# Kernel optimization log

Measured on AMD Instinct MI355X. Metric: run time of the kernel, lower is better.

## Reference

```python
import jax, jax.numpy as jnp
import numpy as np

NEG_SLOPE = 0.2
RECON_W = 0.1
BN_EPS = 1e-5


def gat_conv(x, edge_index, W, a_src, a_dst, b):
    """PyG-style GATConv (eval mode, add_self_loops=True, concat heads).
    x: [N, F_in], W: [F_in, H*C], a_src/a_dst: [H, C], b: [H*C]."""
    N = x.shape[0]
    H, C = a_src.shape
    h = (x @ W).reshape(N, H, C)                      # [N,H,C]
    loop = jnp.arange(N, dtype=edge_index.dtype)
    src = jnp.concatenate([edge_index[0], loop])
    dst = jnp.concatenate([edge_index[1], loop])
    alpha_src = jnp.sum(h * a_src, axis=-1)           # [N,H]
    alpha_dst = jnp.sum(h * a_dst, axis=-1)           # [N,H]
    e = jax.nn.leaky_relu(alpha_src[src] + alpha_dst[dst], NEG_SLOPE)  # [E,H]
    # segment softmax over incoming edges of each destination node
    m = jax.ops.segment_max(e, dst, num_segments=N)
    e = jnp.exp(e - m[dst])
    s = jax.ops.segment_sum(e, dst, num_segments=N)
    p = e / s[dst]                                    # [E,H]
    out = jax.ops.segment_sum(p[:, :, None] * h[src], dst, num_segments=N)  # [N,H,C]
    return out.reshape(N, H * C) + b


def setup_inputs() -> dict:
    key = jax.random.key(0)
    ks = jax.random.split(key, 24)
    N, E = 100000, 800000
    F_in, hid, heads, n_cls, ctx_d, expl_d = 128, 32, 4, 10, 6, 32
    HC = hid * heads  # 128
    g = lambda k, shp, sc=0.1: jax.random.normal(k, shp, dtype=jnp.float32) * sc
    return {
        "x": jax.random.normal(ks[0], (N, F_in), dtype=jnp.float32),
        "edge_index": jax.random.randint(ks[1], (2, E), 0, N, dtype=jnp.int32),
        "context": jax.random.normal(ks[2], (N, ctx_d), dtype=jnp.float32),
        # GATConv 1: F_in -> hid, heads
        "W1": g(ks[3], (F_in, HC)), "a_src1": g(ks[4], (heads, hid)),
        "a_dst1": g(ks[5], (heads, hid)), "b1": g(ks[6], (HC,)),
        # BatchNorm1d(HC), eval mode
        "bn_gamma": jnp.ones((HC,), jnp.float32), "bn_beta": g(ks[7], (HC,)),
        "bn_mean": g(ks[8], (HC,)), "bn_var": jax.random.uniform(ks[9], (HC,), jnp.float32, 0.5, 1.5),
        # GATConv 2: HC -> hid, 1 head
        "W2": g(ks[10], (HC, hid)), "a_src2": g(ks[11], (1, hid)),
        "a_dst2": g(ks[12], (1, hid)), "b2": g(ks[13], (hid,)),
        # Reasoner MLP: ctx_d -> hid -> expl_d
        "rw1": g(ks[14], (ctx_d, hid)), "rb1": g(ks[15], (hid,)),
        "rw2": g(ks[16], (hid, expl_d)), "rb2": g(ks[17], (expl_d,)),
        # Decoder: expl_d -> hid
        "dw": g(ks[18], (expl_d, hid)), "db": g(ks[19], (hid,)),
        # Classifier: hid -> n_cls
        "cw": g(ks[20], (hid, n_cls)), "cb": g(ks[21], (n_cls,)),
    }


def reference(x, edge_index, context, W1, a_src1, a_dst1, b1,
              bn_gamma, bn_beta, bn_mean, bn_var,
              W2, a_src2, a_dst2, b2, rw1, rb1, rw2, rb2, dw, db, cw, cb):
    # layer 1: GAT -> BN(eval) -> ELU (dropout inactive in eval)
    h = gat_conv(x, edge_index, W1, a_src1, a_dst1, b1)
    h = (h - bn_mean) * jax.lax.rsqrt(bn_var + BN_EPS) * bn_gamma + bn_beta
    h = jax.nn.elu(h)
    # layer 2: GAT (1 head)
    h = gat_conv(h, edge_index, W2, a_src2, a_dst2, b2)  # [N, hid]
    # reasoner + decoder
    expl = jnp.maximum(context @ rw1 + rb1, 0.0) @ rw2 + rb2   # [N, expl_d]
    recon = expl @ dw + db                                     # [N, hid]
    combined = h + RECON_W * recon
    logits = combined @ cw + cb
    return jax.nn.log_softmax(logits, axis=1), expl
```

## Files before the change

### kernel.cpp

```cpp
#include <hip/hip_runtime.h>
#include <hip/hip_bf16.h>
#include <math.h>

#define NEG_SLOPE 0.2f
#define RECON_W 0.1f
#define BN_EPS 1e-5f
#define CAP 64

typedef __attribute__((ext_vector_type(8))) short short8;
typedef __attribute__((ext_vector_type(4))) float f32x4;

__device__ __forceinline__ float lrelu(float v) {
    return (v >= 0.f) ? v : NEG_SLOPE * v;
}
__device__ __forceinline__ unsigned short f2bf(float f) {
    unsigned int u = __float_as_uint(f);
    u = (u + 0x7fffu + ((u >> 16) & 1u)) >> 16;
    return (unsigned short)u;
}
__device__ __forceinline__ float bf2f(unsigned short u) {
    return __uint_as_float(((unsigned int)u) << 16);
}
__device__ __forceinline__ unsigned int pack2bf(float a, float b) {
    return (unsigned int)f2bf(a) | ((unsigned int)f2bf(b) << 16);
}
__device__ __forceinline__ void unpack2(unsigned int u, float& a, float& b) {
    a = bf2f((unsigned short)u);
    b = bf2f((unsigned short)(u >> 16));
}

__global__ void bucket_kernel(const int* __restrict__ src, const int* __restrict__ dst, int E,
                              int* __restrict__ cnt, int* __restrict__ csrS) {
    int e = blockIdx.x * blockDim.x + threadIdx.x;
    if (e >= E) return;
    int s = src[e], d = dst[e];
    int pos = atomicAdd(&cnt[d], 1);
    if (pos < CAP) csrS[(size_t)d * CAP + pos] = s;
}

__global__ __launch_bounds__(256) void prep_kernel(
    const float* __restrict__ W1, const float* __restrict__ W2,
    const float* __restrict__ b1, const float* __restrict__ g,
    const float* __restrict__ be, const float* __restrict__ m, const float* __restrict__ v,
    unsigned short* __restrict__ w1t, unsigned short* __restrict__ w2t,
    float* __restrict__ bnsc, float* __restrict__ bnsh) {
    int b = blockIdx.x, tid = threadIdx.x;
    if (b < 64) {
        int e = b * 256 + tid;
        w1t[e] = f2bf(W1[(e & 127) * 128 + (e >> 7)]);
    } else {
        #pragma unroll
        for (int it = 0; it < 16; it++) {
            int e = it * 256 + tid;
            w2t[e] = f2bf(W2[(e & 127) * 32 + (e >> 7)]);
        }
        if (tid < 128) {
            float s = rsqrtf(v[tid] + BN_EPS) * g[tid];
            bnsc[tid] = s;
            bnsh[tid] = (b1[tid] - m[tid]) * s + be[tid];
        }
    }
}

__global__ __launch_bounds__(256) void gemm1_mfma_kernel(
    const float* __restrict__ x, const unsigned short* __restrict__ w1t,
    const float* __restrict__ a_src, const float* __restrict__ a_dst,
    unsigned short* __restrict__ h1g, float* __restrict__ as1, float* __restrict__ ad1, int N) {
    __shared__ unsigned short sA[64 * 128];
    __shared__ unsigned short sBt[128 * 128];
    __shared__ float s_as[128], s_ad[128];
    int tid = threadIdx.x;
    int rowBase = blockIdx.x * 64;

    if (tid < 128) { s_as[tid] = a_src[tid]; s_ad[tid] = a_dst[tid]; }
    #pragma unroll
    for (int u = 0; u < 8; u++) {
        int f = tid + u * 256;
        int r = f >> 5, cg = f & 31;
        int gr = rowBase + r;
        float4 vv = make_float4(0.f, 0.f, 0.f, 0.f);
        if (gr < N) vv = *(const float4*)(x + (size_t)gr * 128 + cg * 4);
        uint2 pk;
        pk.x = pack2bf(vv.x, vv.y);
        pk.y = pack2bf(vv.z, vv.w);
        ((uint2*)sA)[f] = pk;
    }
    #pragma unroll
    for (int u = 0; u < 8; u++) {
        int f = tid + u * 256;
        ((uint4*)sBt)[f] = ((const uint4*)w1t)[f];
    }
    __syncthreads();

    int lane = tid & 63;
    int w = tid >> 6;
    int quad = lane >> 4;
    int m16 = lane & 15;

    f32x4 acc[8];
    #pragma unroll
    for (int t = 0; t < 8; t++) acc[t] = (f32x4){0.f, 0.f, 0.f, 0.f};

    #pragma unroll
    for (int kc = 0; kc < 4; kc++) {
        int k0 = kc * 32 + quad * 8;
        short8 af = *(const short8*)(sA + ((w * 16 + m16) * 128 + k0));
        #pragma unroll
        for (int t = 0; t < 8; t++) {
            short8 bf = *(const short8*)(sBt + ((t * 16 + m16) * 128 + k0));
            acc[t] = __builtin_amdgcn_mfma_f32_16x16x32_bf16(af, bf, acc[t], 0, 0, 0);
        }
    }

    #pragma unroll
    for (int t = 0; t < 8; t++) {
        #pragma unroll
        for (int r = 0; r < 4; r++) {
            int row = w * 16 + quad * 4 + r;
            int col = t * 16 + m16;
            sA[row * 128 + col] = f2bf(acc[t][r]);
        }
    }
    __syncthreads();
    #pragma unroll
    for (int u = 0; u < 8; u++) {
        int f = tid + u * 256;
        int r = f >> 5, cg = f & 31;
        int gr = rowBase + r;
        if (gr < N) *(uint2*)(h1g + (size_t)gr * 128 + cg * 4) = ((const uint2*)sA)[f];
    }
    {
        int row = tid >> 2, head = tid & 3;
        int gr = rowBase + row;
        if (gr < N) {
            const unsigned int* rowp = (const unsigned int*)(sA + row * 128);
            float ps = 0.f, pd = 0.f;
            #pragma unroll
            for (int j = 0; j < 16; j++) {
                float f0, f1;
                unpack2(rowp[head * 16 + j], f0, f1);
                int c = head * 32 + j * 2;
                ps = fmaf(f0, s_as[c], fmaf(f1, s_as[c + 1], ps));
                pd = fmaf(f0, s_ad[c], fmaf(f1, s_ad[c + 1], pd));
            }
            as1[gr * 4 + head] = ps;
            ad1[gr * 4 + head] = pd;
        }
    }
}

__global__ __launch_bounds__(256) void agg1_kernel(
    const unsigned short* __restrict__ h1g,
    const float* __restrict__ as1, const float* __restrict__ ad1,
    const int* __restrict__ cnt, const int* __restrict__ csrS,
    const float* __restrict__ bnscale, const float* __restrict__ bnshift,
    unsigned short* __restrict__ h1p, int N) {
    __shared__ int   sSrc[4][CAP + 2];
    __shared__ float sW[4][CAP + 2][4];
    int tid = threadIdx.x;
    int wid = tid >> 6;
    int lane = tid & 63;
    int n = (int)(((unsigned)blockIdx.x * blockDim.x + tid) >> 6);
    bool alive = (n < N);
    int total = 1;

    if (alive) {
        int deg = min(cnt[n], CAP);
        total = deg + 1;
        float4 ad4 = *(const float4*)(ad1 + (size_t)n * 4);
        if (lane <= deg) {
            int s = (lane < deg) ? csrS[n * CAP + lane] : n;
            float4 a = *(const float4*)(as1 + (size_t)s * 4);
            sSrc[wid][lane] = s;
            float4 w4;
            w4.x = __expf(lrelu(a.x + ad4.x));
            w4.y = __expf(lrelu(a.y + ad4.y));
            w4.z = __expf(lrelu(a.z + ad4.z));
            w4.w = __expf(lrelu(a.w + ad4.w));
            *(float4*)(&sW[wid][lane][0]) = w4;
        }
        if (deg == CAP && lane == 63) {
            float4 a = *(const float4*)(as1 + (size_t)n * 4);
            sSrc[wid][CAP] = n;
            float4 w4;
            w4.x = __expf(lrelu(a.x + ad4.x));
            w4.y = __expf(lrelu(a.y + ad4.y));
            w4.z = __expf(lrelu(a.z + ad4.z));
            w4.w = __expf(lrelu(a.w + ad4.w));
            *(float4*)(&sW[wid][CAP][0]) = w4;
        }
    }
    __syncthreads();
    if (!alive) return;

    int half = lane >> 5;
    int l = lane & 31;
    int hl = l >> 3;
    unsigned choff = (unsigned)(l << 2);
    const int* sS = sSrc[wid];
    const float* sWp = &sW[wid][0][0];

    float p0a = 0.f, p1a = 0.f, p2a = 0.f, p3a = 0.f, sa = 0.f;
    float p0b = 0.f, p1b = 0.f, p2b = 0.f, p3b = 0.f, sb = 0.f;
    int j = half;
    for (; j + 2 < total; j += 4) {
        int s0 = sS[j];
        int s1 = sS[j + 2];
        float w0 = sWp[(j << 2) + hl];
        float w1 = sWp[((j + 2) << 2) + hl];
        uint2 u0 = *(const uint2*)(h1g + (((unsigned)s0 << 7) + choff));
        uint2 u1 = *(const uint2*)(h1g + (((unsigned)s1 << 7) + choff));
        float f0, f1, f2, f3;
        unpack2(u0.x, f0, f1); unpack2(u0.y, f2, f3);
        p0a = fmaf(w0, f0, p0a); p1a = fmaf(w0, f1, p1a);
        p2a = fmaf(w0, f2, p2a); p3a = fmaf(w0, f3, p3a);
        sa += w0;
        unpack2(u1.x, f0, f1); unpack2(u1.y, f2, f3);
        p0b = fmaf(w1, f0, p0b); p1b = fmaf(w1, f1, p1b);
        p2b = fmaf(w1, f2, p2b); p3b = fmaf(w1, f3, p3b);
        sb += w1;
    }
    if (j < total) {
        int s0 = sS[j];
        float w0 = sWp[(j << 2) + hl];
        uint2 u0 = *(const uint2*)(h1g + (((unsigned)s0 << 7) + choff));
        float f0, f1, f2, f3;
        unpack2(u0.x, f0, f1); unpack2(u0.y, f2, f3);
        p0a = fmaf(w0, f0, p0a); p1a = fmaf(w0, f1, p1a);
        p2a = fmaf(w0, f2, p2a); p3a = fmaf(w0, f3, p3a);
        sa += w0;
    }
    float acc0 = p0a + p0b, acc1 = p1a + p1b, acc2 = p2a + p2b, acc3 = p3a + p3b;
    float ss = sa + sb;
    acc0 += __shfl_xor(acc0, 32); acc1 += __shfl_xor(acc1, 32);
    acc2 += __shfl_xor(acc2, 32); acc3 += __shfl_xor(acc3, 32);
    ss += __shfl_xor(ss, 32);
    if (half == 0) {
        float inv = 1.f / ss;
        float4 sc = *(const float4*)(bnscale + l * 4);
        float4 sh = *(const float4*)(bnshift + l * 4);
        float o0 = fmaf(acc0 * inv, sc.x, sh.x);
        float o1 = fmaf(acc1 * inv, sc.y, sh.y);
        float o2 = fmaf(acc2 * inv, sc.z, sh.z);
        float o3 = fmaf(acc3 * inv, sc.w, sh.w);
        o0 = (o0 > 0.f) ? o0 : expm1f(o0);
        o1 = (o1 > 0.f) ? o1 : expm1f(o1);
        o2 = (o2 > 0.f) ? o2 : expm1f(o2);
        o3 = (o3 > 0.f) ? o3 : expm1f(o3);
        uint2 pk;
        pk.x = pack2bf(o0, o1);
        pk.y = pack2bf(o2, o3);
        *(uint2*)(h1p + (size_t)n * 128 + l * 4) = pk;
    }
}

__global__ __launch_bounds__(256) void gemm2_mfma_kernel(
    const unsigned short* __restrict__ A, const unsigned short* __restrict__ w2t,
    const float* __restrict__ a_src, const float* __restrict__ a_dst,
    unsigned short* __restrict__ h2g, float* __restrict__ as2, float* __restrict__ ad2, int N) {
    __shared__ unsigned short sA[64 * 128];
    __shared__ unsigned short sBt[32 * 128];
    __shared__ unsigned short sC[64 * 32];
    __shared__ float s_as[32], s_ad[32];
    int tid = threadIdx.x;
    int rowBase = blockIdx.x * 64;

    if (tid < 32) { s_as[tid] = a_src[tid]; s_ad[tid] = a_dst[tid]; }
    #pragma unroll
    for (int u = 0; u < 4; u++) {
        int f = tid + u * 256;
        int r = f >> 4, g = f & 15;
        int gr = rowBase + r;
        uint4 vv = make_uint4(0, 0, 0, 0);
        if (gr < N) vv = *(const uint4*)(A + (size_t)gr * 128 + g * 8);
        ((uint4*)sA)[f] = vv;
    }
    #pragma unroll
    for (int u = 0; u < 2; u++) {
        int f = tid + u * 256;
        ((uint4*)sBt)[f] = ((const uint4*)w2t)[f];
    }
    __syncthreads();

    int lane = tid & 63;
    int w = tid >> 6;
    int quad = lane >> 4;
    int m16 = lane & 15;

    f32x4 acc[2];
    acc[0] = (f32x4){0.f, 0.f, 0.f, 0.f};
    acc[1] = (f32x4){0.f, 0.f, 0.f, 0.f};
    #pragma unroll
    for (int kc = 0; kc < 4; kc++) {
        int k0 = kc * 32 + quad * 8;
        short8 af = *(const short8*)(sA + ((w * 16 + m16) * 128 + k0));
        #pragma unroll
        for (int t = 0; t < 2; t++) {
            short8 bf = *(const short8*)(sBt + ((t * 16 + m16) * 128 + k0));
            acc[t] = __builtin_amdgcn_mfma_f32_16x16x32_bf16(af, bf, acc[t], 0, 0, 0);
        }
    }
    #pragma unroll
    for (int t = 0; t < 2; t++) {
        #pragma unroll
        for (int r = 0; r < 4; r++) {
            int row = w * 16 + quad * 4 + r;
            sC[row * 32 + t * 16 + m16] = f2bf(acc[t][r]);
        }
    }
    __syncthreads();
    {
        int r = tid >> 2, g = tid & 3;
        int gr = rowBase + r;
        if (gr < N) *(uint4*)(h2g + (size_t)gr * 32 + g * 8) = ((const uint4*)sC)[tid];
    }
    if (tid < 64) {
        int gr = rowBase + tid;
        if (gr < N) {
            const unsigned int* rowp = (const unsigned int*)(sC + tid * 32);
            float ps = 0.f, pd = 0.f;
            #pragma unroll
            for (int j = 0; j < 16; j++) {
                float f0, f1;
                unpack2(rowp[j], f0, f1);
                ps = fmaf(f0, s_as[j * 2], fmaf(f1, s_as[j * 2 + 1], ps));
                pd = fmaf(f0, s_ad[j * 2], fmaf(f1, s_ad[j * 2 + 1], pd));
            }
            as2[gr] = ps;
            ad2[gr] = pd;
        }
    }
}

__global__ __launch_bounds__(256) void agg2_kernel(
    const unsigned short* __restrict__ h2g,
    const float* __restrict__ as2, const float* __restrict__ ad2,
    const int* __restrict__ cnt, const int* __restrict__ csrS,
    const float* __restrict__ b2, float* __restrict__ hl2, int N) {
    __shared__ int   sSrc[4][CAP + 2];
    __shared__ float sW[4][CAP + 2];
    int tid = threadIdx.x;
    int wid = tid >> 6;
    int lane = tid & 63;
    int n = (int)(((unsigned)blockIdx.x * blockDim.x + tid) >> 6);
    bool alive = (n < N);
    int total = 1;

    if (alive) {
        int deg = min(cnt[n], CAP);
        total = deg + 1;
        float ad = ad2[n];
        if (lane <= deg) {
            int s = (lane < deg) ? csrS[n * CAP + lane] : n;
            sSrc[wid][lane] = s;
            sW[wid][lane] = __expf(lrelu(as2[s] + ad));
        }
        if (deg == CAP && lane == 63) {
            sSrc[wid][CAP] = n;
            sW[wid][CAP] = __expf(lrelu(as2[n] + ad));
        }
    }
    __syncthreads();
    if (!alive) return;

    int q = lane >> 4;
    int l = lane & 15;
    unsigned choff = (unsigned)(l << 1);
    const int* sS = sSrc[wid];
    const float* sWp = sW[wid];

    float a0a = 0.f, a1a = 0.f, sa = 0.f;
    float a0b = 0.f, a1b = 0.f, sb = 0.f;
    int j = q;
    for (; j + 4 < total; j += 8) {
        int s0 = sS[j];
        int s1 = sS[j + 4];
        float w0 = sWp[j];
        float w1 = sWp[j + 4];
        unsigned int u0 = *(const unsigned int*)(h2g + (((unsigned)s0 << 5) + choff));
        unsigned int u1 = *(const unsigned int*)(h2g + (((unsigned)s1 << 5) + choff));
        float f0, f1;
        unpack2(u0, f0, f1);
        a0a = fmaf(w0, f0, a0a); a1a = fmaf(w0, f1, a1a); sa += w0;
        unpack2(u1, f0, f1);
        a0b = fmaf(w1, f0, a0b); a1b = fmaf(w1, f1, a1b); sb += w1;
    }
    if (j < total) {
        int s0 = sS[j];
        float w0 = sWp[j];
        unsigned int u0 = *(const unsigned int*)(h2g + (((unsigned)s0 << 5) + choff));
        float f0, f1;
        unpack2(u0, f0, f1);
        a0a = fmaf(w0, f0, a0a); a1a = fmaf(w0, f1, a1a); sa += w0;
    }
    float acc0 = a0a + a0b, acc1 = a1a + a1b, ss = sa + sb;
    acc0 += __shfl_xor(acc0, 16); acc1 += __shfl_xor(acc1, 16); ss += __shfl_xor(ss, 16);
    acc0 += __shfl_xor(acc0, 32); acc1 += __shfl_xor(acc1, 32); ss += __shfl_xor(ss, 32);
    if (lane < 16) {
        float inv = 1.f / ss;
        float2 o = make_float2(acc0 * inv + b2[l * 2], acc1 * inv + b2[l * 2 + 1]);
        *(float2*)(hl2 + (size_t)n * 32 + l * 2) = o;
    }
}

__global__ __launch_bounds__(256) void head_kernel(
    const float* __restrict__ context, const float* __restrict__ hl2,
    const float* __restrict__ rw1, const float* __restrict__ rb1,
    const float* __restrict__ rw2, const float* __restrict__ rb2,
    const float* __restrict__ dw, const float* __restrict__ db,
    const float* __restrict__ cw, const float* __restrict__ cb,
    float* __restrict__ out_lsm, float* __restrict__ out_expl, int N) {
    __shared__ float s_rw1[192], s_rw2[1024], s_dw[1024], s_cw[320];
    __shared__ float s_rb1[32], s_rb2[32], s_db[32], s_cb[10];
    int tid = threadIdx.x;
    for (int i = tid; i < 192; i += 256) s_rw1[i] = rw1[i];
    for (int i = tid; i < 1024; i += 256) { s_rw2[i] = rw2[i]; s_dw[i] = dw[i]; }
    for (int i = tid; i < 320; i += 256) s_cw[i] = cw[i];
    if (tid < 32) { s_rb1[tid] = rb1[tid]; s_rb2[tid] = rb2[tid]; s_db[tid] = db[tid]; }
    if (tid < 10) s_cb[tid] = cb[tid];
    __syncthreads();
    int n = blockIdx.x * 256 + tid;
    if (n >= N) return;

    float ctx[6];
    #pragma unroll
    for (int i = 0; i < 6; i++) ctx[i] = context[(size_t)n * 6 + i];

    float t1[32];
    #pragma unroll
    for (int c = 0; c < 32; c++) t1[c] = s_rb1[c];
    #pragma unroll
    for (int i = 0; i < 6; i++) {
        float s = ctx[i];
        #pragma unroll
        for (int c = 0; c < 32; c++) t1[c] = fmaf(s, s_rw1[i * 32 + c], t1[c]);
    }
    #pragma unroll
    for (int c = 0; c < 32; c++) t1[c] = fmaxf(t1[c], 0.f);

    float ex[32];
    #pragma unroll
    for (int c = 0; c < 32; c++) ex[c] = s_rb2[c];
    #pragma unroll
    for (int c = 0; c < 32; c++) {
        float s = t1[c];
        #pragma unroll
        for (int c2 = 0; c2 < 32; c2++) ex[c2] = fmaf(s, s_rw2[c * 32 + c2], ex[c2]);
    }
    #pragma unroll
    for (int c = 0; c < 32; c += 4)
        *(float4*)(out_expl + (size_t)n * 32 + c) = make_float4(ex[c], ex[c + 1], ex[c + 2], ex[c + 3]);

    float rec[32];
    #pragma unroll
    for (int k = 0; k < 32; k++) rec[k] = s_db[k];
    #pragma unroll
    for (int c = 0; c < 32; c++) {
        float s = ex[c];
        #pragma unroll
        for (int k = 0; k < 32; k++) rec[k] = fmaf(s, s_dw[c * 32 + k], rec[k]);
    }
    float comb[32];
    #pragma unroll
    for (int k = 0; k < 32; k += 4) {
        float4 h = *(const float4*)(hl2 + (size_t)n * 32 + k);
        comb[k] = h.x + RECON_W * rec[k];
        comb[k + 1] = h.y + RECON_W * rec[k + 1];
        comb[k + 2] = h.z + RECON_W * rec[k + 2];
        comb[k + 3] = h.w + RECON_W * rec[k + 3];
    }
    float lg[10];
    #pragma unroll
    for (int j = 0; j < 10; j++) lg[j] = s_cb[j];
    #pragma unroll
    for (int k = 0; k < 32; k++) {
        float s = comb[k];
        #pragma unroll
        for (int j = 0; j < 10; j++) lg[j] = fmaf(s, s_cw[k * 10 + j], lg[j]);
    }
    float mx = lg[0];
    #pragma unroll
    for (int j = 1; j < 10; j++) mx = fmaxf(mx, lg[j]);
    float se = 0.f;
    #pragma unroll
    for (int j = 0; j < 10; j++) se += expf(lg[j] - mx);
    float lse = mx + logf(se);
    #pragma unroll
    for (int j = 0; j < 10; j++) out_lsm[(size_t)n * 10 + j] = lg[j] - lse;
}

extern "C" void kernel_launch(void* const* d_in, const int* in_sizes, int n_in,
                              void* d_out, int out_size, void* d_ws, size_t ws_size,
                              hipStream_t stream) {
    const float* x    = (const float*)d_in[0];
    const int* ei     = (const int*)d_in[1];
    const float* ctx  = (const float*)d_in[2];
    const float* W1   = (const float*)d_in[3];
    const float* a_s1 = (const float*)d_in[4];
    const float* a_d1 = (const float*)d_in[5];
    const float* b1   = (const float*)d_in[6];
    const float* bn_g = (const float*)d_in[7];
    const float* bn_b = (const float*)d_in[8];
    const float* bn_m = (const float*)d_in[9];
    const float* bn_v = (const float*)d_in[10];
    const float* W2   = (const float*)d_in[11];
    const float* a_s2 = (const float*)d_in[12];
    const float* a_d2 = (const float*)d_in[13];
    const float* b2   = (const float*)d_in[14];
    const float* rw1  = (const float*)d_in[15];
    const float* rb1  = (const float*)d_in[16];
    const float* rw2  = (const float*)d_in[17];
    const float* rb2  = (const float*)d_in[18];
    const float* dw   = (const float*)d_in[19];
    const float* db   = (const float*)d_in[20];
    const float* cw   = (const float*)d_in[21];
    const float* cb   = (const float*)d_in[22];

    int N = in_sizes[0] / 128;
    int E = in_sizes[1] / 2;
    const int* esrc = ei;
    const int* edst = ei + E;

    char* w = (char*)d_ws;
    auto alloc = [&](size_t bytes) {
        void* p = (void*)w;
        w += (bytes + 255) & ~(size_t)255;
        return p;
    };
    unsigned short* h1g = (unsigned short*)alloc((size_t)N * 128 * 2);
    unsigned short* h1p = (unsigned short*)alloc((size_t)N * 128 * 2);
    float* as1  = (float*)alloc((size_t)N * 4 * 4);
    float* ad1  = (float*)alloc((size_t)N * 4 * 4);
    float* as2  = (float*)alloc((size_t)N * 4);
    float* ad2  = (float*)alloc((size_t)N * 4);
    int* cnt    = (int*)alloc((size_t)N * 4);
    int* csrS   = (int*)alloc((size_t)N * CAP * 4);
    float* bnsc = (float*)alloc(128 * 4);
    float* bnsh = (float*)alloc(128 * 4);
    unsigned short* w1t = (unsigned short*)alloc(128 * 128 * 2);
    unsigned short* w2t = (unsigned short*)alloc(32 * 128 * 2);
    unsigned short* h2g = h1g;
    float* hl2 = (float*)(h1g + (size_t)N * 32);

    float* out0 = (float*)d_out;
    float* out1 = out0 + (size_t)N * 10;

    hipMemsetAsync(cnt, 0, (size_t)N * 4, stream);

    bucket_kernel<<<(E + 255) / 256, 256, 0, stream>>>(esrc, edst, E, cnt, csrS);
    prep_kernel<<<65, 256, 0, stream>>>(W1, W2, b1, bn_g, bn_b, bn_m, bn_v,
                                        w1t, w2t, bnsc, bnsh);
    gemm1_mfma_kernel<<<(N + 63) / 64, 256, 0, stream>>>(x, w1t, a_s1, a_d1, h1g, as1, ad1, N);
    agg1_kernel<<<(N + 3) / 4, 256, 0, stream>>>(h1g, as1, ad1, cnt, csrS,
                                                 bnsc, bnsh, h1p, N);
    gemm2_mfma_kernel<<<(N + 63) / 64, 256, 0, stream>>>(h1p, w2t, a_s2, a_d2, h2g, as2, ad2, N);
    agg2_kernel<<<(N + 3) / 4, 256, 0, stream>>>(h2g, as2, ad2, cnt, csrS, b2, hl2, N);
    head_kernel<<<(N + 255) / 256, 256, 0, stream>>>(ctx, hl2, rw1, rb1, rw2, rb2,
                                                     dw, db, cw, cb, out0, out1, N);
}
```

Measured before the change: 338.6 us.

## Assign fewer lanes per node in GAT aggregation kernels with wider loads

Both aggregation kernels now map a small lane group to each destination node (16 lanes in layer one, 8 in layer two) rather than a full 64-lane wavefront. Each lane loads wider vectors (uint4 / uint2) and keeps more accumulators, which removes the cross-half shuffle reductions. Since the average degree is about 9, this is meant to cut idle lanes and per-node overhead. The cost is more registers per thread and a serial edge loop inside each group, which can diverge when degrees differ within a wavefront.

```diff
diff --git a/kernel.cpp b/kernel.cpp
--- a/kernel.cpp
+++ b/kernel.cpp
@@ -155,103 +155,102 @@
     const int* __restrict__ cnt, const int* __restrict__ csrS,
     const float* __restrict__ bnscale, const float* __restrict__ bnshift,
     unsigned short* __restrict__ h1p, int N) {
-    __shared__ int   sSrc[4][CAP + 2];
-    __shared__ float sW[4][CAP + 2][4];
+    __shared__ int   sSrc[16][CAP + 1];
+    __shared__ float sW[16][CAP + 1][4];
     int tid = threadIdx.x;
-    int wid = tid >> 6;
-    int lane = tid & 63;
-    int n = (int)(((unsigned)blockIdx.x * blockDim.x + tid) >> 6);
+    int nid = tid >> 4;
+    int l   = tid & 15;
+    int n = blockIdx.x * 16 + nid;
     bool alive = (n < N);
-    int total = 1;
+    int total = 0;
 
     if (alive) {
         int deg = min(cnt[n], CAP);
         total = deg + 1;
         float4 ad4 = *(const float4*)(ad1 + (size_t)n * 4);
-        if (lane <= deg) {
-            int s = (lane < deg) ? csrS[n * CAP + lane] : n;
+        for (int slot = l; slot < total; slot += 16) {
+            int s = (slot < deg) ? csrS[n * CAP + slot] : n;
+            sSrc[nid][slot] = s;
             float4 a = *(const float4*)(as1 + (size_t)s * 4);
-            sSrc[wid][lane] = s;
             float4 w4;
             w4.x = __expf(lrelu(a.x + ad4.x));
             w4.y = __expf(lrelu(a.y + ad4.y));
             w4.z = __expf(lrelu(a.z + ad4.z));
             w4.w = __expf(lrelu(a.w + ad4.w));
-            *(float4*)(&sW[wid][lane][0]) = w4;
-        }
-        if (deg == CAP && lane == 63) {
-            float4 a = *(const float4*)(as1 + (size_t)n * 4);
-            sSrc[wid][CAP] = n;
-            float4 w4;
-            w4.x = __expf(lrelu(a.x + ad4.x));
-            w4.y = __expf(lrelu(a.y + ad4.y));
-            w4.z = __expf(lrelu(a.z + ad4.z));
-            w4.w = __expf(lrelu(a.w + ad4.w));
-            *(float4*)(&sW[wid][CAP][0]) = w4;
+            *(float4*)(&sW[nid][slot][0]) = w4;
         }
     }
     __syncthreads();
     if (!alive) return;
 
-    int half = lane >> 5;
-    int l = lane & 31;
-    int hl = l >> 3;
-    unsigned choff = (unsigned)(l << 2);
-    const int* sS = sSrc[wid];
-    const float* sWp = &sW[wid][0][0];
-
-    float p0a = 0.f, p1a = 0.f, p2a = 0.f, p3a = 0.f, sa = 0.f;
-    float p0b = 0.f, p1b = 0.f, p2b = 0.f, p3b = 0.f, sb = 0.f;
-    int j = half;
-    for (; j + 2 < total; j += 4) {
+    int hl = l >> 2;
+    unsigned choff = (unsigned)(l << 3);
+    const int* sS = sSrc[nid];
+    const float* sWp = &sW[nid][0][0];
+
+    float pa0 = 0.f, pa1 = 0.f, pa2 = 0.f, pa3 = 0.f;
+    float pa4 = 0.f, pa5 = 0.f, pa6 = 0.f, pa7 = 0.f;
+    float pb0 = 0.f, pb1 = 0.f, pb2 = 0.f, pb3 = 0.f;
+    float pb4 = 0.f, pb5 = 0.f, pb6 = 0.f, pb7 = 0.f;
+    float sa = 0.f, sb = 0.f;
+    int j = 0;
+    for (; j + 1 < total; j += 2) {
         int s0 = sS[j];
-        int s1 = sS[j + 2];
+        int s1 = sS[j + 1];
         float w0 = sWp[(j << 2) + hl];
-        float w1 = sWp[((j + 2) << 2) + hl];
-        uint2 u0 = *(const uint2*)(h1g + (((unsigned)s0 << 7) + choff));
-        uint2 u1 = *(const uint2*)(h1g + (((unsigned)s1 << 7) + choff));
-        float f0, f1, f2, f3;
-        unpack2(u0.x, f0, f1); unpack2(u0.y, f2, f3);
-        p0a = fmaf(w0, f0, p0a); p1a = fmaf(w0, f1, p1a);
-        p2a = fmaf(w0, f2, p2a); p3a = fmaf(w0, f3, p3a);
+        float w1 = sWp[((j + 1) << 2) + hl];
+        uint4 u0 = *(const uint4*)(h1g + (((unsigned)s0 << 7) + choff));
+        uint4 u1 = *(const uint4*)(h1g + (((unsigned)s1 << 7) + choff));
+        float f0, f1;
+        unpack2(u0.x, f0, f1); pa0 = fmaf(w0, f0, pa0); pa1 = fmaf(w0, f1, pa1);
+        unpack2(u0.y, f0, f1); pa2 = fmaf(w0, f0, pa2); pa3 = fmaf(w0, f1, pa3);
+        unpack2(u0.z, f0, f1); pa4 = fmaf(w0, f0, pa4); pa5 = fmaf(w0, f1, pa5);
+        unpack2(u0.w, f0, f1); pa6 = fmaf(w0, f0, pa6); pa7 = fmaf(w0, f1, pa7);
         sa += w0;
-        unpack2(u1.x, f0, f1); unpack2(u1.y, f2, f3);
-        p0b = fmaf(w1, f0, p0b); p1b = fmaf(w1, f1, p1b);
-        p2b = fmaf(w1, f2, p2b); p3b = fmaf(w1, f3, p3b);
+        unpack2(u1.x, f0, f1); pb0 = fmaf(w1, f0, pb0); pb1 = fmaf(w1, f1, pb1);
+        unpack2(u1.y, f0, f1); pb2 = fmaf(w1, f0, pb2); pb3 = fmaf(w1, f1, pb3);
+        unpack2(u1.z, f0, f1); pb4 = fmaf(w1, f0, pb4); pb5 = fmaf(w1, f1, pb5);
+        unpack2(u1.w, f0, f1); pb6 = fmaf(w1, f0, pb6); pb7 = fmaf(w1, f1, pb7);
         sb += w1;
     }
     if (j < total) {
         int s0 = sS[j];
         float w0 = sWp[(j << 2) + hl];
-        uint2 u0 = *(const uint2*)(h1g + (((unsigned)s0 << 7) + choff));
-        float f0, f1, f2, f3;
-        unpack2(u0.x, f0, f1); unpack2(u0.y, f2, f3);
-        p0a = fmaf(w0, f0, p0a); p1a = fmaf(w0, f1, p1a);
-        p2a = fmaf(w0, f2, p2a); p3a = fmaf(w0, f3, p3a);
+        uint4 u0 = *(const uint4*)(h1g + (((unsigned)s0 << 7) + choff));
+        float f0, f1;
+        unpack2(u0.x, f0, f1); pa0 = fmaf(w0, f0, pa0); pa1 = fmaf(w0, f1, pa1);
+        unpack2(u0.y, f0, f1); pa2 = fmaf(w0, f0, pa2); pa3 = fmaf(w0, f1, pa3);
+        unpack2(u0.z, f0, f1); pa4 = fmaf(w0, f0, pa4); pa5 = fmaf(w0, f1, pa5);
+        unpack2(u0.w, f0, f1); pa6 = fmaf(w0, f0, pa6); pa7 = fmaf(w0, f1, pa7);
         sa += w0;
     }
-    float acc0 = p0a + p0b, acc1 = p1a + p1b, acc2 = p2a + p2b, acc3 = p3a + p3b;
-    float ss = sa + sb;
-    acc0 += __shfl_xor(acc0, 32); acc1 += __shfl_xor(acc1, 32);
-    acc2 += __shfl_xor(acc2, 32); acc3 += __shfl_xor(acc3, 32);
-    ss += __shfl_xor(ss, 32);
-    if (half == 0) {
-        float inv = 1.f / ss;
-        float4 sc = *(const float4*)(bnscale + l * 4);
-        float4 sh = *(const float4*)(bnshift + l * 4);
-        float o0 = fmaf(acc0 * inv, sc.x, sh.x);
-        float o1 = fmaf(acc1 * inv, sc.y, sh.y);
-        float o2 = fmaf(acc2 * inv, sc.z, sh.z);
-        float o3 = fmaf(acc3 * inv, sc.w, sh.w);
-        o0 = (o0 > 0.f) ? o0 : expm1f(o0);
-        o1 = (o1 > 0.f) ? o1 : expm1f(o1);
-        o2 = (o2 > 0.f) ? o2 : expm1f(o2);
-        o3 = (o3 > 0.f) ? o3 : expm1f(o3);
-        uint2 pk;
-        pk.x = pack2bf(o0, o1);
-        pk.y = pack2bf(o2, o3);
-        *(uint2*)(h1p + (size_t)n * 128 + l * 4) = pk;
-    }
+    float inv = 1.f / (sa + sb);
+    float4 sc0 = *(const float4*)(bnscale + l * 8);
+    float4 sc1 = *(const float4*)(bnscale + l * 8 + 4);
+    float4 sh0 = *(const float4*)(bnshift + l * 8);
+    float4 sh1 = *(const float4*)(bnshift + l * 8 + 4);
+    float o0 = fmaf((pa0 + pb0) * inv, sc0.x, sh0.x);
+    float o1 = fmaf((pa1 + pb1) * inv, sc0.y, sh0.y);
+    float o2 = fmaf((pa2 + pb2) * inv, sc0.z, sh0.z);
+    float o3 = fmaf((pa3 + pb3) * inv, sc0.w, sh0.w);
+    float o4 = fmaf((pa4 + pb4) * inv, sc1.x, sh1.x);
+    float o5 = fmaf((pa5 + pb5) * inv, sc1.y, sh1.y);
+    float o6 = fmaf((pa6 + pb6) * inv, sc1.z, sh1.z);
+    float o7 = fmaf((pa7 + pb7) * inv, sc1.w, sh1.w);
+    o0 = (o0 > 0.f) ? o0 : expm1f(o0);
+    o1 = (o1 > 0.f) ? o1 : expm1f(o1);
+    o2 = (o2 > 0.f) ? o2 : expm1f(o2);
+    o3 = (o3 > 0.f) ? o3 : expm1f(o3);
+    o4 = (o4 > 0.f) ? o4 : expm1f(o4);
+    o5 = (o5 > 0.f) ? o5 : expm1f(o5);
+    o6 = (o6 > 0.f) ? o6 : expm1f(o6);
+    o7 = (o7 > 0.f) ? o7 : expm1f(o7);
+    uint4 pk;
+    pk.x = pack2bf(o0, o1);
+    pk.y = pack2bf(o2, o3);
+    pk.z = pack2bf(o4, o5);
+    pk.w = pack2bf(o6, o7);
+    *(uint4*)(h1p + (size_t)n * 128 + l * 8) = pk;
 }
 
 __global__ __launch_bounds__(256) void gemm2_mfma_kernel(
@@ -337,70 +336,67 @@
     const float* __restrict__ as2, const float* __restrict__ ad2,
     const int* __restrict__ cnt, const int* __restrict__ csrS,
     const float* __restrict__ b2, float* __restrict__ hl2, int N) {
-    __shared__ int   sSrc[4][CAP + 2];
-    __shared__ float sW[4][CAP + 2];
+    __shared__ int   sSrc[32][CAP + 1];
+    __shared__ float sW[32][CAP + 1];
     int tid = threadIdx.x;
-    int wid = tid >> 6;
-    int lane = tid & 63;
-    int n = (int)(((unsigned)blockIdx.x * blockDim.x + tid) >> 6);
+    int nid = tid >> 3;
+    int l   = tid & 7;
+    int n = blockIdx.x * 32 + nid;
     bool alive = (n < N);
-    int total = 1;
+    int total = 0;
 
     if (alive) {
         int deg = min(cnt[n], CAP);
         total = deg + 1;
         float ad = ad2[n];
-        if (lane <= deg) {
-            int s = (lane < deg) ? csrS[n * CAP + lane] : n;
-            sSrc[wid][lane] = s;
-            sW[wid][lane] = __expf(lrelu(as2[s] + ad));
-        }
-        if (deg == CAP && lane == 63) {
-            sSrc[wid][CAP] = n;
-            sW[wid][CAP] = __expf(lrelu(as2[n] + ad));
+        for (int slot = l; slot < total; slot += 8) {
+            int s = (slot < deg) ? csrS[n * CAP + slot] : n;
+            sSrc[nid][slot] = s;
+            sW[nid][slot] = __expf(lrelu(as2[s] + ad));
         }
     }
     __syncthreads();
     if (!alive) return;
 
-    int q = lane >> 4;
-    int l = lane & 15;
-    unsigned choff = (unsigned)(l << 1);
-    const int* sS = sSrc[wid];
-    const float* sWp = sW[wid];
-
-    float a0a = 0.f, a1a = 0.f, sa = 0.f;
-    float a0b = 0.f, a1b = 0.f, sb = 0.f;
-    int j = q;
-    for (; j + 4 < total; j += 8) {
+    unsigned choff = (unsigned)(l << 2);
+    const int* sS = sSrc[nid];
+    const float* sWp = sW[nid];
+
+    float a0a = 0.f, a1a = 0.f, a2a = 0.f, a3a = 0.f, sa = 0.f;
+    float a0b = 0.f, a1b = 0.f, a2b = 0.f, a3b = 0.f, sb = 0.f;
+    int j = 0;
+    for (; j + 1 < total; j += 2) {
         int s0 = sS[j];
-        int s1 = sS[j + 4];
+        int s1 = sS[j + 1];
         float w0 = sWp[j];
-        float w1 = sWp[j + 4];
-        unsigned int u0 = *(const unsigned int*)(h2g + (((unsigned)s0 << 5) + choff));
-        unsigned int u1 = *(const unsigned int*)(h2g + (((unsigned)s1 << 5) + choff));
+        float w1 = sWp[j + 1];
+        uint2 u0 = *(const uint2*)(h2g + (((unsigned)s0 << 5) + choff));
+        uint2 u1 = *(const uint2*)(h2g + (((unsigned)s1 << 5) + choff));
         float f0, f1;
-        unpack2(u0, f0, f1);
-        a0a = fmaf(w0, f0, a0a); a1a = fmaf(w0, f1, a1a); sa += w0;
-        unpack2(u1, f0, f1);
-        a0b = fmaf(w1, f0, a0b); a1b = fmaf(w1, f1, a1b); sb += w1;
+        unpack2(u0.x, f0, f1); a0a = fmaf(w0, f0, a0a); a1a = fmaf(w0, f1, a1a);
+        unpack2(u0.y, f0, f1); a2a = fmaf(w0, f0, a2a); a3a = fmaf(w0, f1, a3a);
+        sa += w0;
+        unpack2(u1.x, f0, f1); a0b = fmaf(w1, f0, a0b); a1b = fmaf(w1, f1, a1b);
+        unpack2(u1.y, f0, f1); a2b = fmaf(w1, f0, a2b); a3b = fmaf(w1, f1, a3b);
+        sb += w1;
     }
     if (j < total) {
         int s0 = sS[j];
         float w0 = sWp[j];
-        unsigned int u0 = *(const unsigned int*)(h2g + (((unsigned)s0 << 5) + choff));
+        uint2 u0 = *(const uint2*)(h2g + (((unsigned)s0 << 5) + choff));
         float f0, f1;
-        unpack2(u0, f0, f1);
-        a0a = fmaf(w0, f0, a0a); a1a = fmaf(w0, f1, a1a); sa += w0;
-    }
-    float acc0 = a0a + a0b, acc1 = a1a + a1b, ss = sa + sb;
-    acc0 += __shfl_xor(acc0, 16); acc1 += __shfl_xor(acc1, 16); ss += __shfl_xor(ss, 16);
-    acc0 += __shfl_xor(acc0, 32); acc1 += __shfl_xor(acc1, 32); ss += __shfl_xor(ss, 32);
-    if (lane < 16) {
-        float inv = 1.f / ss;
-        float2 o = make_float2(acc0 * inv + b2[l * 2], acc1 * inv + b2[l * 2 + 1]);
-        *(float2*)(hl2 + (size_t)n * 32 + l * 2) = o;
-    }
+        unpack2(u0.x, f0, f1); a0a = fmaf(w0, f0, a0a); a1a = fmaf(w0, f1, a1a);
+        unpack2(u0.y, f0, f1); a2a = fmaf(w0, f0, a2a); a3a = fmaf(w0, f1, a3a);
+        sa += w0;
+    }
+    float inv = 1.f / (sa + sb);
+    float4 bb = *(const float4*)(b2 + l * 4);
+    float4 o;
+    o.x = (a0a + a0b) * inv + bb.x;
+    o.y = (a1a + a1b) * inv + bb.y;
+    o.z = (a2a + a2b) * inv + bb.z;
+    o.w = (a3a + a3b) * inv + bb.w;
+    *(float4*)(hl2 + (size_t)n * 32 + l * 4) = o;
 }
 
 __global__ __launch_bounds__(256) void head_kernel(
@@ -551,10 +547,10 @@
     prep_kernel<<<65, 256, 0, stream>>>(W1, W2, b1, bn_g, bn_b, bn_m, bn_v,
                                         w1t, w2t, bnsc, bnsh);
     gemm1_mfma_kernel<<<(N + 63) / 64, 256, 0, stream>>>(x, w1t, a_s1, a_d1, h1g, as1, ad1, N);
-    agg1_kernel<<<(N + 3) / 4, 256, 0, stream>>>(h1g, as1, ad1, cnt, csrS,
-                                                 bnsc, bnsh, h1p, N);
+    agg1_kernel<<<(N + 15) / 16, 256, 0, stream>>>(h1g, as1, ad1, cnt, csrS,
+                                                   bnsc, bnsh, h1p, N);
     gemm2_mfma_kernel<<<(N + 63) / 64, 256, 0, stream>>>(h1p, w2t, a_s2, a_d2, h2g, as2, ad2, N);
-    agg2_kernel<<<(N + 3) / 4, 256, 0, stream>>>(h2g, as2, ad2, cnt, csrS, b2, hl2, N);
+    agg2_kernel<<<(N + 31) / 32, 256, 0, stream>>>(h2g, as2, ad2, cnt, csrS, b2, hl2, N);
     head_kernel<<<(N + 255) / 256, 256, 0, stream>>>(ctx, hl2, rw1, rb1, rw2, rb2,
                                                      dw, db, cw, cb, out0, out1, N);
 }
```

After: 310.6 us. -8.3%, faster.
